# Kernel tuning notes

Measured on AMD Instinct MI355X. Metric: run time of the kernel, lower is better.

The kernel has to match this reference:

```python
import jax, jax.numpy as jnp
import numpy as np

EPS = 1e-8      # torch F.cosine_similarity eps
MARGIN = 0.6
POS_MASK = 2.0  # added at the positive location before top-k mining
K_NEG = 4


def setup_inputs() -> dict:
    key = jax.random.key(0)
    k1, k2, k3, k4 = jax.random.split(key, 4)
    B, C, H, W = 4, 256, 64, 64
    sketch = jax.random.normal(k1, (B, C, H, W), dtype=jnp.float32)
    ref = jax.random.normal(k2, (B, C, H, W), dtype=jnp.float32)
    # one anchor coordinate per positive grid cell (B*H*W pairs total)
    anchor_y = jax.random.randint(k3, (B, H * W), 0, H, dtype=jnp.int32)
    anchor_x = jax.random.randint(k4, (B, H * W), 0, W, dtype=jnp.int32)
    return {"sketch_query_vectors": sketch, "ref_key_vectors": ref,
            "anchor_y": anchor_y, "anchor_x": anchor_x}


def reference(sketch_query_vectors, ref_key_vectors, anchor_y, anchor_x):
    B, C, H, W = sketch_query_vectors.shape
    M = H * W  # ref locations; also number of positive pairs per batch elem

    sketch_flat = sketch_query_vectors.reshape(B, C, M)  # (B, C, M)
    ref_flat = ref_key_vectors.reshape(B, C, M)          # (B, C, M)

    # gather anchor features at (anchor_y, anchor_x): flat index ay*W + ax
    a_idx = anchor_y * W + anchor_x                      # (B, N), N == M
    anchors = jnp.take_along_axis(sketch_flat, a_idx[:, None, :], axis=2)  # (B, C, N)
    anchors = anchors.transpose(0, 2, 1)                 # (B, N, C)

    # cosine similarity of each anchor vs full ref map of same batch elem
    dot = jnp.einsum('bnc,bcm->bnm', anchors, ref_flat)  # (B, N, M)
    a_norm = jnp.linalg.norm(anchors, axis=-1)           # (B, N)
    r_norm = jnp.linalg.norm(ref_flat, axis=1)           # (B, M)
    sim = dot / jnp.maximum(a_norm[:, :, None] * r_norm[:, None, :], EPS)
    dist = 1.0 - sim                                     # (B, N, M)

    # positive location for pair n is grid cell n -> diagonal
    pos_distance = jnp.mean(jnp.diagonal(dist, axis1=1, axis2=2))

    # mask the positive location then mine 4 smallest distances
    masked = dist + POS_MASK * jnp.eye(M, dtype=dist.dtype)[None, :, :]
    neg_vals = -jax.lax.top_k(-masked, K_NEG)[0]         # (B, N, K_NEG)
    neg_loss = jnp.mean(jnp.maximum(MARGIN - neg_vals, 0.0))

    return pos_distance + neg_loss
```

## Files before the change

### kernel.cpp

```cpp
#include <hip/hip_runtime.h>
#include <math.h>

#define B_  4
#define C_  256
#define W_  64
#define M_  4096
#define N_  4096
#define THRESH_ 0.4f

typedef __attribute__((ext_vector_type(8))) short bf16x8;
typedef __attribute__((ext_vector_type(4))) float f32x4;

__device__ __forceinline__ short f2bf(float x) {
    union { float f; unsigned u; } v; v.f = x;
    unsigned r = v.u + 0x7fffu + ((v.u >> 16) & 1u);
    return (short)(r >> 16);
}
__device__ __forceinline__ float bf2f(short s) {
    union { unsigned u; float f; } v;
    v.u = ((unsigned)(unsigned short)s) << 16;
    return v.f;
}
__device__ __forceinline__ void gload_lds16(const void* g, void* l) {
    __builtin_amdgcn_global_load_lds(
        (const __attribute__((address_space(1))) void*)g,
        (__attribute__((address_space(3))) void*)l, 16, 0, 0);
}

#define OFF_SKT    0
#define OFF_REFT   8388608
#define OFF_ISN    16777216
#define OFF_IR     16842752
#define OFF_SSUM   16908288
#define OFF_DIAG   16908288
#define OFF_ROWSUM 16973824
#define OFF_ROWCNT 17039360
#define OFF_FLAGC  17104896
#define OFF_FLAGL  17105152
#define OFF_AIDX   17170688

__global__ __launch_bounds__(256) void convert_kernel(
    const float* __restrict__ sketch, const float* __restrict__ ref,
    short* __restrict__ sketchT, short* __restrict__ refT,
    float* __restrict__ ssum)
{
    const int b  = blockIdx.x >> 4;
    const int m  = (blockIdx.x & 15) * 256 + threadIdx.x;
    const int cq = blockIdx.y;
    const int z  = blockIdx.z;

    const float* src = (z ? ref : sketch) + ((size_t)(b * C_ + cq * 64)) * M_ + m;
    short* dst = (z ? refT : sketchT) + ((size_t)(b * M_ + m)) * C_ + cq * 64;

    float ss = 0.f;
#pragma unroll
    for (int j8 = 0; j8 < 8; ++j8) {
        bf16x8 v;
#pragma unroll
        for (int e = 0; e < 8; ++e) {
            float x = src[(size_t)(j8 * 8 + e) * M_];
            ss += x * x;
            v[e] = f2bf(x);
        }
        *reinterpret_cast<bf16x8*>(dst + j8 * 8) = v;
    }
    ssum[(size_t)(z * 4 + cq) * (B_ * M_) + b * M_ + m] = ss;
}

__global__ __launch_bounds__(256) void fin_kernel(
    const float* __restrict__ ssum, float* __restrict__ isn,
    float* __restrict__ ir)
{
    const int i = blockIdx.x * 256 + threadIdx.x;
    float s0 = 0.f, s1 = 0.f;
#pragma unroll
    for (int cq = 0; cq < 4; ++cq) {
        s0 += ssum[(size_t)cq * (B_ * M_) + i];
        s1 += ssum[(size_t)(4 + cq) * (B_ * M_) + i];
    }
    isn[i] = rsqrtf(s0);
    ir[i]  = rsqrtf(s1);
}

__global__ __launch_bounds__(256) void prep2_kernel(
    const int* __restrict__ ay, const int* __restrict__ ax,
    int* __restrict__ aidx, float* __restrict__ rowsum,
    int* __restrict__ rowcnt, int* __restrict__ flagcnt)
{
    const int i = blockIdx.x * 256 + threadIdx.x;
    aidx[i] = ay[i] * W_ + ax[i];
    rowsum[i] = 0.f;
    rowcnt[i] = 0;
    if (i == 0) *flagcnt = 0;
}

#define BK 64

__global__ __launch_bounds__(256) void gemm_kernel(
    const short* __restrict__ sketchT, const short* __restrict__ refT,
    const int* __restrict__ aidx,
    const float* __restrict__ isn, const float* __restrict__ ir,
    float* __restrict__ diag, float* __restrict__ rowsum,
    int* __restrict__ rowcnt)
{
    const int mBase = blockIdx.x * 128;
    const int nBase = blockIdx.y * 128;
    const int b = blockIdx.z;
    const int tid = threadIdx.x;
    const int lane = tid & 63, wv = tid >> 6;
    const int wm = (wv >> 1) * 64, wn = (wv & 1) * 64;
    const int l15 = lane & 15, l4 = lane >> 4;
    const int l7 = lane & 7, l8 = lane >> 3;
    const int ksw = ((l7 ^ l8) << 3);

    __shared__ __align__(16) short Rs[128 * BK];
    __shared__ __align__(16) short As[128 * BK];

    const short* asrc[4];
    const short* bsrc[4];
#pragma unroll
    for (int c = 0; c < 4; ++c) {
        const int row = (wv * 4 + c) * 8 + l8;
        asrc[c] = refT + ((size_t)b * M_ + mBase + row) * C_ + ksw;
        const int an = aidx[b * N_ + nBase + row];
        bsrc[c] = sketchT + ((size_t)b * M_ + an) * C_ + ksw;
    }

    f32x4 acc[4][4] = {};

    for (int k0 = 0; k0 < C_; k0 += BK) {
#pragma unroll
        for (int c = 0; c < 4; ++c) {
            const int cb = wv * 4 + c;
            gload_lds16(asrc[c] + k0, (char*)Rs + cb * 1024);
            gload_lds16(bsrc[c] + k0, (char*)As + cb * 1024);
        }
        __syncthreads();

#pragma unroll
        for (int ks = 0; ks < 2; ++ks) {
            bf16x8 pm[4], pn[4];
#pragma unroll
            for (int f = 0; f < 4; ++f) {
                const int rowA = wm + f * 16 + l15;
                const int rowB = wn + f * 16 + l15;
                const int kphys = ((ks * 4 + l4) ^ (l15 & 7)) << 3;
                pm[f] = *reinterpret_cast<const bf16x8*>(&Rs[rowA * BK + kphys]);
                pn[f] = *reinterpret_cast<const bf16x8*>(&As[rowB * BK + kphys]);
            }
#pragma unroll
            for (int fi = 0; fi < 4; ++fi)
#pragma unroll
                for (int fj = 0; fj < 4; ++fj)
                    acc[fi][fj] = __builtin_amdgcn_mfma_f32_16x16x32_bf16(
                        pm[fi], pn[fj], acc[fi][fj], 0, 0, 0);
        }
        __syncthreads();
    }

    float irv[4][4];
#pragma unroll
    for (int fi = 0; fi < 4; ++fi)
#pragma unroll
        for (int r = 0; r < 4; ++r)
            irv[fi][r] = ir[b * M_ + mBase + wm + fi * 16 + l4 * 4 + r];

#pragma unroll
    for (int fj = 0; fj < 4; ++fj) {
        const int gn = nBase + wn + fj * 16 + l15;
        const float ian = isn[b * M_ + aidx[b * N_ + gn]];
        float s = 0.f; int cnt = 0;
#pragma unroll
        for (int fi = 0; fi < 4; ++fi) {
#pragma unroll
            for (int r = 0; r < 4; ++r) {
                const int gm = mBase + wm + fi * 16 + l4 * 4 + r;
                const float sim = acc[fi][fj][r] * irv[fi][r] * ian;
                if (gm == gn) {
                    diag[b * N_ + gn] = 1.0f - sim;
                } else if (sim > THRESH_) {
                    s += sim - THRESH_; ++cnt;
                }
            }
        }
        if (cnt) {
            atomicAdd(&rowsum[b * N_ + gn], s);
            atomicAdd(&rowcnt[b * N_ + gn], cnt);
        }
    }
}

__global__ __launch_bounds__(256) void flag_kernel(
    const int* __restrict__ rowcnt, int* __restrict__ flagcnt,
    int* __restrict__ flaglist)
{
    int i = blockIdx.x * 256 + threadIdx.x;
    if (rowcnt[i] > 4) {
        int p = atomicAdd(flagcnt, 1);
        flaglist[p] = i;
    }
}

__global__ __launch_bounds__(256) void fallback_kernel(
    const short* __restrict__ sketchT, const short* __restrict__ refT,
    const int* __restrict__ aidx,
    const float* __restrict__ isn, const float* __restrict__ ir,
    const int* __restrict__ flagcnt, const int* __restrict__ flaglist,
    float* __restrict__ rowsum)
{
    const int nflag = *flagcnt;
    __shared__ float av[C_];
    __shared__ float tops[256][4];
    for (int fi = blockIdx.x; fi < nflag; fi += gridDim.x) {
        const int row = flaglist[fi];
        const int b = row >> 12, n = row & (N_ - 1);
        const int an = aidx[row];
        __syncthreads();
        av[threadIdx.x] = bf2f(sketchT[((size_t)b * M_ + an) * C_ + threadIdx.x]);
        __syncthreads();
        const float ian = isn[b * M_ + an];
        float t0 = 0, t1 = 0, t2 = 0, t3 = 0;
        for (int m = threadIdx.x; m < M_; m += 256) {
            if (m == n) continue;
            const short* rp = refT + ((size_t)b * M_ + m) * C_;
            float dot = 0.f;
#pragma unroll 8
            for (int c = 0; c < C_; ++c) dot += av[c] * bf2f(rp[c]);
            float rl = dot * ian * ir[b * M_ + m] - THRESH_;
            if (rl > t3) {
                t3 = rl;
                if (t3 > t2) { float t = t2; t2 = t3; t3 = t; }
                if (t2 > t1) { float t = t1; t1 = t2; t2 = t; }
                if (t1 > t0) { float t = t0; t0 = t1; t1 = t; }
            }
        }
        tops[threadIdx.x][0] = t0; tops[threadIdx.x][1] = t1;
        tops[threadIdx.x][2] = t2; tops[threadIdx.x][3] = t3;
        __syncthreads();
        if (threadIdx.x == 0) {
            float s0 = 0, s1 = 0, s2 = 0, s3 = 0;
            for (int t = 0; t < 1024; ++t) {
                float v = tops[t >> 2][t & 3];
                if (v > s3) {
                    s3 = v;
                    if (s3 > s2) { float tt = s2; s2 = s3; s3 = tt; }
                    if (s2 > s1) { float tt = s1; s1 = s2; s2 = tt; }
                    if (s1 > s0) { float tt = s0; s0 = s1; s1 = tt; }
                }
            }
            rowsum[row] = s0 + s1 + s2 + s3;
        }
        __syncthreads();
    }
}

__global__ __launch_bounds__(256) void final_kernel(
    const float* __restrict__ rowsum, const float* __restrict__ diag,
    float* __restrict__ out)
{
    float sn = 0.f, sp = 0.f;
    for (int i = threadIdx.x; i < B_ * N_; i += 256) {
        sn += rowsum[i];
        sp += diag[i];
    }
    __shared__ float red[256];
    red[threadIdx.x] = sp * (1.0f / (B_ * N_)) + sn * (1.0f / (B_ * N_ * 4));
    __syncthreads();
    for (int s = 128; s > 0; s >>= 1) {
        if (threadIdx.x < s) red[threadIdx.x] += red[threadIdx.x + s];
        __syncthreads();
    }
    if (threadIdx.x == 0) out[0] = red[0];
}

extern "C" void kernel_launch(void* const* d_in, const int* in_sizes, int n_in,
                              void* d_out, int out_size, void* d_ws, size_t ws_size,
                              hipStream_t stream)
{
    const float* sketch = (const float*)d_in[0];
    const float* ref    = (const float*)d_in[1];
    const int*   ay     = (const int*)d_in[2];
    const int*   ax     = (const int*)d_in[3];
    float* out = (float*)d_out;

    char* ws = (char*)d_ws;
    short* sketchT  = (short*)(ws + OFF_SKT);
    short* refT     = (short*)(ws + OFF_REFT);
    float* isn      = (float*)(ws + OFF_ISN);
    float* ir       = (float*)(ws + OFF_IR);
    float* ssum     = (float*)(ws + OFF_SSUM);
    float* diag     = (float*)(ws + OFF_DIAG);
    float* rowsum   = (float*)(ws + OFF_ROWSUM);
    int*   rowcnt   = (int*)(ws + OFF_ROWCNT);
    int*   flagcnt  = (int*)(ws + OFF_FLAGC);
    int*   flaglist = (int*)(ws + OFF_FLAGL);
    int*   aidx     = (int*)(ws + OFF_AIDX);

    convert_kernel<<<dim3(16 * B_, 4, 2), 256, 0, stream>>>(
        sketch, ref, sketchT, refT, ssum);
    fin_kernel<<<(B_ * M_) / 256, 256, 0, stream>>>(ssum, isn, ir);
    prep2_kernel<<<(B_ * N_) / 256, 256, 0, stream>>>(
        ay, ax, aidx, rowsum, rowcnt, flagcnt);

    gemm_kernel<<<dim3(M_ / 128, N_ / 128, B_), 256, 0, stream>>>(
        sketchT, refT, aidx, isn, ir, diag, rowsum, rowcnt);

    flag_kernel<<<(B_ * N_) / 256, 256, 0, stream>>>(rowcnt, flagcnt, flaglist);
    fallback_kernel<<<64, 256, 0, stream>>>(sketchT, refT, aidx, isn, ir,
                                            flagcnt, flaglist, rowsum);
    final_kernel<<<1, 256, 0, stream>>>(rowsum, diag, out);
}
```

Before: 156.3 us.

## Enlarge GEMM tile to 256x256 with double-buffered LDS pipeline and fuse prep kernels

The GEMM moves from 128x128 tiles with 4 waves to 256x256 tiles with 8 waves. It double-buffers LDS, prefetching the next K slice while MFMAs run, and uses s_setprio and a block-index swizzle for cache locality. Small kernels are merged: fin and prep2 become finprep, the convert kernel covers 128 channels per block, and flag_kernel is dropped. In its place, fallback_kernel scans rowcnt over all rows itself. The aim is less launch overhead and more reuse per tile, at the cost of heavier register and LDS use (128KB of LDS per block), and the fallback must now scan every row.

```diff
diff --git a/kernel.cpp b/kernel.cpp
--- a/kernel.cpp
+++ b/kernel.cpp
@@ -32,12 +32,10 @@
 #define OFF_ISN    16777216
 #define OFF_IR     16842752
 #define OFF_SSUM   16908288
-#define OFF_DIAG   16908288
-#define OFF_ROWSUM 16973824
-#define OFF_ROWCNT 17039360
-#define OFF_FLAGC  17104896
-#define OFF_FLAGL  17105152
-#define OFF_AIDX   17170688
+#define OFF_DIAG   17170432
+#define OFF_ROWSUM 17235968
+#define OFF_ROWCNT 17301504
+#define OFF_AIDX   17367040
 
 __global__ __launch_bounds__(256) void convert_kernel(
     const float* __restrict__ sketch, const float* __restrict__ ref,
@@ -46,15 +44,15 @@
 {
     const int b  = blockIdx.x >> 4;
     const int m  = (blockIdx.x & 15) * 256 + threadIdx.x;
-    const int cq = blockIdx.y;
+    const int ch = blockIdx.y;
     const int z  = blockIdx.z;
 
-    const float* src = (z ? ref : sketch) + ((size_t)(b * C_ + cq * 64)) * M_ + m;
-    short* dst = (z ? refT : sketchT) + ((size_t)(b * M_ + m)) * C_ + cq * 64;
+    const float* src = (z ? ref : sketch) + ((size_t)(b * C_ + ch * 128)) * M_ + m;
+    short* dst = (z ? refT : sketchT) + ((size_t)(b * M_ + m)) * C_ + ch * 128;
 
     float ss = 0.f;
 #pragma unroll
-    for (int j8 = 0; j8 < 8; ++j8) {
+    for (int j8 = 0; j8 < 16; ++j8) {
         bf16x8 v;
 #pragma unroll
         for (int e = 0; e < 8; ++e) {
@@ -64,118 +62,144 @@
         }
         *reinterpret_cast<bf16x8*>(dst + j8 * 8) = v;
     }
-    ssum[(size_t)(z * 4 + cq) * (B_ * M_) + b * M_ + m] = ss;
-}
-
-__global__ __launch_bounds__(256) void fin_kernel(
-    const float* __restrict__ ssum, float* __restrict__ isn,
-    float* __restrict__ ir)
+    ssum[(size_t)(z * 2 + ch) * (B_ * M_) + b * M_ + m] = ss;
+}
+
+__global__ __launch_bounds__(256) void finprep_kernel(
+    const float* __restrict__ ssum,
+    const int* __restrict__ ay, const int* __restrict__ ax,
+    float* __restrict__ isn, float* __restrict__ ir,
+    int* __restrict__ aidx, float* __restrict__ rowsum,
+    int* __restrict__ rowcnt)
 {
     const int i = blockIdx.x * 256 + threadIdx.x;
-    float s0 = 0.f, s1 = 0.f;
-#pragma unroll
-    for (int cq = 0; cq < 4; ++cq) {
-        s0 += ssum[(size_t)cq * (B_ * M_) + i];
-        s1 += ssum[(size_t)(4 + cq) * (B_ * M_) + i];
-    }
-    isn[i] = rsqrtf(s0);
-    ir[i]  = rsqrtf(s1);
-}
-
-__global__ __launch_bounds__(256) void prep2_kernel(
-    const int* __restrict__ ay, const int* __restrict__ ax,
-    int* __restrict__ aidx, float* __restrict__ rowsum,
-    int* __restrict__ rowcnt, int* __restrict__ flagcnt)
-{
-    const int i = blockIdx.x * 256 + threadIdx.x;
+    isn[i] = rsqrtf(ssum[i] + ssum[B_ * M_ + i]);
+    ir[i]  = rsqrtf(ssum[2 * B_ * M_ + i] + ssum[3 * B_ * M_ + i]);
     aidx[i] = ay[i] * W_ + ax[i];
     rowsum[i] = 0.f;
     rowcnt[i] = 0;
-    if (i == 0) *flagcnt = 0;
 }
 
 #define BK 64
-
-__global__ __launch_bounds__(256) void gemm_kernel(
+#define NT 4
+
+__global__ __launch_bounds__(512, 2) void gemm_kernel(
     const short* __restrict__ sketchT, const short* __restrict__ refT,
     const int* __restrict__ aidx,
     const float* __restrict__ isn, const float* __restrict__ ir,
     float* __restrict__ diag, float* __restrict__ rowsum,
     int* __restrict__ rowcnt)
 {
-    const int mBase = blockIdx.x * 128;
-    const int nBase = blockIdx.y * 128;
-    const int b = blockIdx.z;
+    const int bid = blockIdx.x + (blockIdx.y << 4) + (blockIdx.z << 8);
+    const int nb  = (bid & 7) * 128 + (bid >> 3);
+    const int mBase = (nb & 15) * 256;
+    const int nBase = ((nb >> 4) & 15) * 256;
+    const int b = nb >> 8;
+
     const int tid = threadIdx.x;
     const int lane = tid & 63, wv = tid >> 6;
-    const int wm = (wv >> 1) * 64, wn = (wv & 1) * 64;
+    const int wm = (wv >> 2) * 128;
+    const int wn = (wv & 3) * 64;
     const int l15 = lane & 15, l4 = lane >> 4;
     const int l7 = lane & 7, l8 = lane >> 3;
     const int ksw = ((l7 ^ l8) << 3);
 
-    __shared__ __align__(16) short Rs[128 * BK];
-    __shared__ __align__(16) short As[128 * BK];
-
-    const short* asrc[4];
-    const short* bsrc[4];
+    __shared__ __align__(16) short Rs[2][256 * BK];
+    __shared__ __align__(16) short As[2][256 * BK];
+
+    const short* aptr[4];
+    const short* bptr[4];
 #pragma unroll
     for (int c = 0; c < 4; ++c) {
-        const int row = (wv * 4 + c) * 8 + l8;
-        asrc[c] = refT + ((size_t)b * M_ + mBase + row) * C_ + ksw;
-        const int an = aidx[b * N_ + nBase + row];
-        bsrc[c] = sketchT + ((size_t)b * M_ + an) * C_ + ksw;
-    }
-
-    f32x4 acc[4][4] = {};
-
-    for (int k0 = 0; k0 < C_; k0 += BK) {
-#pragma unroll
-        for (int c = 0; c < 4; ++c) {
-            const int cb = wv * 4 + c;
-            gload_lds16(asrc[c] + k0, (char*)Rs + cb * 1024);
-            gload_lds16(bsrc[c] + k0, (char*)As + cb * 1024);
-        }
-        __syncthreads();
-
-#pragma unroll
-        for (int ks = 0; ks < 2; ++ks) {
-            bf16x8 pm[4], pn[4];
-#pragma unroll
-            for (int f = 0; f < 4; ++f) {
-                const int rowA = wm + f * 16 + l15;
-                const int rowB = wn + f * 16 + l15;
-                const int kphys = ((ks * 4 + l4) ^ (l15 & 7)) << 3;
-                pm[f] = *reinterpret_cast<const bf16x8*>(&Rs[rowA * BK + kphys]);
-                pn[f] = *reinterpret_cast<const bf16x8*>(&As[rowB * BK + kphys]);
+        const int row = wv * 32 + c * 8 + l8;
+        aptr[c] = refT + ((size_t)b * M_ + mBase + row) * C_ + ksw;
+        bptr[c] = sketchT +
+                  ((size_t)b * M_ + aidx[b * N_ + nBase + row]) * C_ + ksw;
+    }
+
+#define STAGE_CHUNK(bufi, c, koff)                                          \
+    gload_lds16(aptr[c] + (koff), (char*)Rs[bufi] + (wv * 4 + (c)) * 1024); \
+    gload_lds16(bptr[c] + (koff), (char*)As[bufi] + (wv * 4 + (c)) * 1024);
+
+    f32x4 acc[8][4] = {};
+    bf16x8 pn[4][2];
+
+#pragma unroll
+    for (int c = 0; c < 4; ++c) { STAGE_CHUNK(0, c, 0) }
+#pragma unroll
+    for (int c = 0; c < 4; ++c) { STAGE_CHUNK(1, c, BK) }
+    asm volatile("s_waitcnt vmcnt(8)" ::: "memory");
+    __builtin_amdgcn_s_barrier();
+
+#pragma unroll
+    for (int t = 0; t < NT; ++t) {
+        const int cur = t & 1;
+        const int koff = (t + 1) * BK;
+#pragma unroll
+        for (int p = 0; p < 4; ++p) {
+            bf16x8 pm[2][2];
+#pragma unroll
+            for (int m2 = 0; m2 < 2; ++m2)
+#pragma unroll
+                for (int ks = 0; ks < 2; ++ks) {
+                    const int row = wm + (p * 2 + m2) * 16 + l15;
+                    const int kph = ((ks * 4 + l4) ^ (l15 & 7)) << 3;
+                    pm[m2][ks] = *reinterpret_cast<const bf16x8*>(
+                        &Rs[cur][row * BK + kph]);
+                }
+            if (p == 0) {
+#pragma unroll
+                for (int nf = 0; nf < 4; ++nf)
+#pragma unroll
+                    for (int ks = 0; ks < 2; ++ks) {
+                        const int row = wn + nf * 16 + l15;
+                        const int kph = ((ks * 4 + l4) ^ (l15 & 7)) << 3;
+                        pn[nf][ks] = *reinterpret_cast<const bf16x8*>(
+                            &As[cur][row * BK + kph]);
+                    }
             }
-#pragma unroll
-            for (int fi = 0; fi < 4; ++fi)
-#pragma unroll
-                for (int fj = 0; fj < 4; ++fj)
-                    acc[fi][fj] = __builtin_amdgcn_mfma_f32_16x16x32_bf16(
-                        pm[fi], pn[fj], acc[fi][fj], 0, 0, 0);
-        }
-        __syncthreads();
-    }
-
-    float irv[4][4];
-#pragma unroll
-    for (int fi = 0; fi < 4; ++fi)
+            if (t == 1 || t == 2) { STAGE_CHUNK(cur ^ 1, p, koff) }
+            __builtin_amdgcn_s_barrier();
+            __builtin_amdgcn_sched_barrier(0);
+            __builtin_amdgcn_s_setprio(1);
+#pragma unroll
+            for (int m2 = 0; m2 < 2; ++m2)
+#pragma unroll
+                for (int nf = 0; nf < 4; ++nf)
+#pragma unroll
+                    for (int ks = 0; ks < 2; ++ks)
+                        acc[p * 2 + m2][nf] =
+                            __builtin_amdgcn_mfma_f32_16x16x32_bf16(
+                                pm[m2][ks], pn[nf][ks],
+                                acc[p * 2 + m2][nf], 0, 0, 0);
+            __builtin_amdgcn_s_setprio(0);
+            if (p < 3) __builtin_amdgcn_s_barrier();
+        }
+        if (t < NT - 1) {
+            asm volatile("s_waitcnt vmcnt(0)" ::: "memory");
+            __builtin_amdgcn_s_barrier();
+        }
+    }
+#undef STAGE_CHUNK
+
+    float irv[8][4];
+#pragma unroll
+    for (int mf = 0; mf < 8; ++mf)
 #pragma unroll
         for (int r = 0; r < 4; ++r)
-            irv[fi][r] = ir[b * M_ + mBase + wm + fi * 16 + l4 * 4 + r];
-
-#pragma unroll
-    for (int fj = 0; fj < 4; ++fj) {
-        const int gn = nBase + wn + fj * 16 + l15;
+            irv[mf][r] = ir[b * M_ + mBase + wm + mf * 16 + l4 * 4 + r];
+
+#pragma unroll
+    for (int nf = 0; nf < 4; ++nf) {
+        const int gn = nBase + wn + nf * 16 + l15;
         const float ian = isn[b * M_ + aidx[b * N_ + gn]];
         float s = 0.f; int cnt = 0;
 #pragma unroll
-        for (int fi = 0; fi < 4; ++fi) {
+        for (int mf = 0; mf < 8; ++mf) {
 #pragma unroll
             for (int r = 0; r < 4; ++r) {
-                const int gm = mBase + wm + fi * 16 + l4 * 4 + r;
-                const float sim = acc[fi][fj][r] * irv[fi][r] * ian;
+                const int gm = mBase + wm + mf * 16 + l4 * 4 + r;
+                const float sim = acc[mf][nf][r] * irv[mf][r] * ian;
                 if (gm == gn) {
                     diag[b * N_ + gn] = 1.0f - sim;
                 } else if (sim > THRESH_) {
@@ -190,29 +214,16 @@
     }
 }
 
-__global__ __launch_bounds__(256) void flag_kernel(
-    const int* __restrict__ rowcnt, int* __restrict__ flagcnt,
-    int* __restrict__ flaglist)
-{
-    int i = blockIdx.x * 256 + threadIdx.x;
-    if (rowcnt[i] > 4) {
-        int p = atomicAdd(flagcnt, 1);
-        flaglist[p] = i;
-    }
-}
-
 __global__ __launch_bounds__(256) void fallback_kernel(
     const short* __restrict__ sketchT, const short* __restrict__ refT,
     const int* __restrict__ aidx,
     const float* __restrict__ isn, const float* __restrict__ ir,
-    const int* __restrict__ flagcnt, const int* __restrict__ flaglist,
-    float* __restrict__ rowsum)
-{
-    const int nflag = *flagcnt;
+    const int* __restrict__ rowcnt, float* __restrict__ rowsum)
+{
     __shared__ float av[C_];
     __shared__ float tops[256][4];
-    for (int fi = blockIdx.x; fi < nflag; fi += gridDim.x) {
-        const int row = flaglist[fi];
+    for (int row = blockIdx.x; row < B_ * N_; row += gridDim.x) {
+        if (rowcnt[row] <= 4) continue;
         const int b = row >> 12, n = row & (N_ - 1);
         const int an = aidx[row];
         __syncthreads();
@@ -292,21 +303,17 @@
     float* diag     = (float*)(ws + OFF_DIAG);
     float* rowsum   = (float*)(ws + OFF_ROWSUM);
     int*   rowcnt   = (int*)(ws + OFF_ROWCNT);
-    int*   flagcnt  = (int*)(ws + OFF_FLAGC);
-    int*   flaglist = (int*)(ws + OFF_FLAGL);
     int*   aidx     = (int*)(ws + OFF_AIDX);
 
-    convert_kernel<<<dim3(16 * B_, 4, 2), 256, 0, stream>>>(
+    convert_kernel<<<dim3(16 * B_, 2, 2), 256, 0, stream>>>(
         sketch, ref, sketchT, refT, ssum);
-    fin_kernel<<<(B_ * M_) / 256, 256, 0, stream>>>(ssum, isn, ir);
-    prep2_kernel<<<(B_ * N_) / 256, 256, 0, stream>>>(
-        ay, ax, aidx, rowsum, rowcnt, flagcnt);
-
-    gemm_kernel<<<dim3(M_ / 128, N_ / 128, B_), 256, 0, stream>>>(
+    finprep_kernel<<<(B_ * M_) / 256, 256, 0, stream>>>(
+        ssum, ay, ax, isn, ir, aidx, rowsum, rowcnt);
+
+    gemm_kernel<<<dim3(16, 16, 4), 512, 0, stream>>>(
         sketchT, refT, aidx, isn, ir, diag, rowsum, rowcnt);
 
-    flag_kernel<<<(B_ * N_) / 256, 256, 0, stream>>>(rowcnt, flagcnt, flaglist);
     fallback_kernel<<<64, 256, 0, stream>>>(sketchT, refT, aidx, isn, ir,
-                                            flagcnt, flaglist, rowsum);
+                                            rowcnt, rowsum);
     final_kernel<<<1, 256, 0, stream>>>(rowsum, diag, out);
 }
```

Measured after the change: 215.9 us. 38.1% more time.
